# Kernel tuning notes

Hardware: AMD Instinct MI355X
Metric: run time of the kernel (lower is better)

## Reference

```python
import jax, jax.numpy as jnp
import numpy as np

EPS = 1e-12   # F.normalize default eps
TH = 0.5      # forward-arg default threshold
CLAMP_LO, CLAMP_HI = 0.01, 0.999


def setup_inputs() -> dict:
    key = jax.random.key(0)
    k1, k2 = jax.random.split(key)
    # x4: ResNet layer3 features after ala1 scaling + upfeat, stride-16 of a 1024px image
    x4 = jax.random.normal(k1, (8, 1024, 64, 64), dtype=jnp.float32)
    # logits: classifier output after upfeat, same spatial grid, 21 classes
    logits = jax.random.normal(k2, (8, 21, 64, 64), dtype=jnp.float32)
    return {"x4": x4, "logits": logits, "pcm": 2}


def reference(x4, logits, pcm):
    b, c, h, w = x4.shape
    hw = h * w
    xf = x4.reshape(b, c, hw)                      # [b, c, hw]
    # F.normalize(dim=1): x / max(||x||_2, eps)
    norm = jnp.sqrt(jnp.sum(xf * xf, axis=1, keepdims=True))
    xn = xf / jnp.maximum(norm, EPS)
    # pixel affinity: [b, hw, hw]
    aff = jnp.einsum('bci,bcj->bij', xn, xn)
    aff = jnp.clip(aff, CLAMP_LO, CLAMP_HI)
    aff = jnp.where(aff < TH, jnp.zeros((), aff.dtype), aff)
    # column-normalize (torch sum over dim=1)
    aff = aff / jnp.sum(aff, axis=1, keepdims=True)
    lf = logits.reshape(b, -1, hw)                 # [b, K, hw]
    for _ in range(pcm):                           # pcm is a Python int
        lf = jnp.einsum('bki,bij->bkj', lf, aff)
    return lf.reshape(b, -1, h, w)
```

## Files before the change

### kernel.cpp

```cpp
#include <hip/hip_runtime.h>
#include <hip/hip_bf16.h>

#define B_   8
#define C_   1024
#define HW_  4096
#define NK   21
#define NT   32
#define NTRI (NT * (NT + 1) / 2)

using bf16 = __hip_bfloat16;
typedef __attribute__((ext_vector_type(4))) float float4_;
typedef __attribute__((ext_vector_type(8))) int int8v;

#define WAITV0() asm volatile("s_waitcnt vmcnt(0)" ::: "memory")
#define FENCE()  asm volatile("" ::: "memory")
#define BARRIER() do { FENCE(); __builtin_amdgcn_s_barrier(); FENCE(); } while (0)

__global__ __launch_bounds__(256) void ktrans(const float* __restrict__ x4, float* __restrict__ sumsq,
                                              unsigned char* __restrict__ Xq, float* __restrict__ colsum) {
    int jt = blockIdx.x, b = blockIdx.y;
    int j0 = jt * 64;
    int t = threadIdx.x;
    __shared__ float tin[128][33];
    __shared__ unsigned int outw[32][260];
    __shared__ float ssq[32];

    if (t < 64) colsum[b * HW_ + j0 + t] = 0.f;

    int jl = t & 31, cl = t >> 5;
    int qq = t >> 5, jq = t & 31;

    for (int jg = 0; jg < 2; ++jg) {
        int jbase = j0 + jg * 32;
        if (t < 32) ssq[t] = 0.f;
        float part = 0.f;

        for (int ct = 0; ct < 8; ++ct) {
            __syncthreads();
#pragma unroll
            for (int cc = 0; cc < 16; ++cc) {
                float v = x4[((size_t)b * C_ + ct * 128 + cc * 8 + cl) * HW_ + jbase + jl];
                tin[cc * 8 + cl][jl] = v;
                part = fmaf(v, v, part);
            }
            __syncthreads();
            unsigned int wv[4];
#pragma unroll
            for (int g = 0; g < 4; ++g) {
                float f0 = tin[qq * 16 + g * 4 + 0][jq];
                float f1 = tin[qq * 16 + g * 4 + 1][jq];
                float f2 = tin[qq * 16 + g * 4 + 2][jq];
                float f3 = tin[qq * 16 + g * 4 + 3][jq];
                unsigned int r = 0;
                r = __builtin_amdgcn_cvt_pk_fp8_f32(f0, f1, r, false);
                r = __builtin_amdgcn_cvt_pk_fp8_f32(f2, f3, r, true);
                wv[g] = r;
            }
            *(uint4*)&outw[jq][ct * 32 + qq * 4] = make_uint4(wv[0], wv[1], wv[2], wv[3]);
        }
        atomicAdd(&ssq[jl], part);
        __syncthreads();

#pragma unroll
        for (int ps = 0; ps < 8; ++ps) {
            int r = ps * 4 + (t >> 6);
            int ch = t & 63;
            uint4 v = *(const uint4*)&outw[r][ch * 4];
            *(uint4*)(Xq + ((size_t)b * HW_ + jbase + r) * C_ + ch * 16) = v;
        }
        if (t < 32) sumsq[b * HW_ + jbase + t] = ssq[t];
        __syncthreads();
    }
}

__global__ __launch_bounds__(256, 2) void kgram(const unsigned char* __restrict__ Xq,
                                                const float* __restrict__ sumsq, bf16* __restrict__ aff,
                                                float* __restrict__ colsum, int* __restrict__ flags) {
    int lin = blockIdx.x;
    int b = lin & 7;
    int p = lin >> 3;
    int it = (int)((2.0f * NT + 1.0f - sqrtf((2.0f * NT + 1.0f) * (2.0f * NT + 1.0f) - 8.0f * (float)p)) * 0.5f);
    while (it > 0 && p < it * NT - it * (it - 1) / 2) --it;
    while (p >= (it + 1) * NT - (it + 1) * it / 2) ++it;
    int jt = it + p - (it * NT - it * (it - 1) / 2);

    int i0 = it * 128, j0 = jt * 128;
    int tid = threadIdx.x, w = tid >> 6, l = tid & 63;
    int wr = w >> 1, wc = w & 1;
    int lrow = l & 15, lk = l >> 4;

    __shared__ __align__(16) unsigned char smem[2][32768];
    __shared__ int fl;

    const unsigned char* XA = Xq + ((size_t)b * HW_ + i0) * C_;
    const unsigned char* XB = Xq + ((size_t)b * HW_ + j0) * C_;

    int rhi = tid >> 3, sl = tid & 7;

    auto stg = [&](unsigned char* buf, int k0) {
#pragma unroll
        for (int q = 0; q < 4; ++q) {
            int R = q * 32 + rhi;
            int gp = sl ^ (R & 7);
            __builtin_amdgcn_global_load_lds(
                (const __attribute__((address_space(1))) void*)(XA + (size_t)R * C_ + k0 + (gp << 4)),
                (__attribute__((address_space(3))) void*)(buf + R * 128 + (sl << 4)), 16, 0, 0);
            __builtin_amdgcn_global_load_lds(
                (const __attribute__((address_space(1))) void*)(XB + (size_t)R * C_ + k0 + (gp << 4)),
                (__attribute__((address_space(3))) void*)(buf + 16384 + R * 128 + (sl << 4)), 16, 0, 0);
        }
    };

    auto ldfrag = [&](const unsigned char* base, int r) {
        int sw = r & 7;
        uint4 lo = *(const uint4*)(base + r * 128 + (((lk * 2) ^ sw) << 4));
        uint4 hi = *(const uint4*)(base + r * 128 + (((lk * 2 + 1) ^ sw) << 4));
        int8v v; v[0] = lo.x; v[1] = lo.y; v[2] = lo.z; v[3] = lo.w;
        v[4] = hi.x; v[5] = hi.y; v[6] = hi.z; v[7] = hi.w;
        return v;
    };

    float4_ acc[4][4];
#pragma unroll
    for (int m = 0; m < 4; ++m)
#pragma unroll
        for (int n = 0; n < 4; ++n) acc[m][n] = {0.f, 0.f, 0.f, 0.f};

    stg(smem[0], 0);
    WAITV0();
    BARRIER();

    for (int kt = 0; kt < 8; ++kt) {
        unsigned char* cur = smem[kt & 1];
        if (kt < 7) stg(smem[(kt + 1) & 1], (kt + 1) * 128);

        int8v bv[4];
#pragma unroll
        for (int n = 0; n < 4; ++n) bv[n] = ldfrag(cur + 16384, wc * 64 + n * 16 + lrow);
        __builtin_amdgcn_s_setprio(1);
#pragma unroll
        for (int m = 0; m < 4; ++m) {
            int8v av = ldfrag(cur, wr * 64 + m * 16 + lrow);
#pragma unroll
            for (int n = 0; n < 4; ++n)
                acc[m][n] = __builtin_amdgcn_mfma_scale_f32_16x16x128_f8f6f4(
                    av, bv[n], acc[m][n], 0, 0, 0, 0x7f7f7f7f, 0, 0x7f7f7f7f);
        }
        __builtin_amdgcn_s_setprio(0);

        if (kt < 7) WAITV0();
        BARRIER();
    }

    float rnj[4];
#pragma unroll
    for (int n = 0; n < 4; ++n) {
        int j = j0 + wc * 64 + n * 16 + lrow;
        rnj[n] = 1.0f / fmaxf(sqrtf(sumsq[b * HW_ + j]), 1e-12f);
    }
    float rni[4][4];
#pragma unroll
    for (int m = 0; m < 4; ++m)
#pragma unroll
        for (int r = 0; r < 4; ++r) {
            int i = i0 + wr * 64 + m * 16 + lk * 4 + r;
            rni[m][r] = 1.0f / fmaxf(sqrtf(sumsq[b * HW_ + i]), 1e-12f);
        }
    bool any = false;
#pragma unroll
    for (int m = 0; m < 4; ++m)
#pragma unroll
        for (int n = 0; n < 4; ++n)
#pragma unroll
            for (int r = 0; r < 4; ++r) {
                acc[m][n][r] *= rni[m][r] * rnj[n];
                any |= (acc[m][n][r] >= 0.5f);
            }

    if (tid == 0) fl = 0;
    __syncthreads();
    unsigned long long bal = __ballot(any);
    if (l == 0 && bal != 0ull) atomicOr(&fl, 1);
    __syncthreads();
    bool mirror = (it != jt);
    if (tid == 0) {
        flags[(b * NT + it) * NT + jt] = fl;
        if (mirror) flags[(b * NT + jt) * NT + it] = fl;
    }

    if (fl) {
        size_t affb = (size_t)b * HW_ * HW_;
        float rsum[4][4];
#pragma unroll
        for (int m = 0; m < 4; ++m)
#pragma unroll
            for (int r = 0; r < 4; ++r) rsum[m][r] = 0.f;

#pragma unroll
        for (int n = 0; n < 4; ++n) {
            int j = j0 + wc * 64 + n * 16 + lrow;
            float cs = 0.f;
#pragma unroll
            for (int m = 0; m < 4; ++m) {
#pragma unroll
                for (int r = 0; r < 4; ++r) {
                    float v = acc[m][n][r];
                    v = fminf(fmaxf(v, 0.01f), 0.999f);
                    v = (v < 0.5f) ? 0.0f : v;
                    bf16 bb = __float2bfloat16(v);
                    int i = i0 + wr * 64 + m * 16 + lk * 4 + r;
                    aff[affb + (size_t)i * HW_ + j] = bb;
                    float bf = __bfloat162float(bb);
                    cs += bf;
                    rsum[m][r] += bf;
                    if (mirror) aff[affb + (size_t)j * HW_ + i] = bb;
                }
            }
            cs += __shfl_xor(cs, 16);
            cs += __shfl_xor(cs, 32);
            if (lk == 0) atomicAdd(&colsum[b * HW_ + j], cs);
        }
        if (mirror) {
#pragma unroll
            for (int m = 0; m < 4; ++m) {
#pragma unroll
                for (int r = 0; r < 4; ++r) {
                    float s = rsum[m][r];
                    s += __shfl_xor(s, 1);
                    s += __shfl_xor(s, 2);
                    s += __shfl_xor(s, 4);
                    s += __shfl_xor(s, 8);
                    if (lrow == 0) {
                        int i = i0 + wr * 64 + m * 16 + lk * 4 + r;
                        atomicAdd(&colsum[b * HW_ + i], s);
                    }
                }
            }
        }
    }
}

__global__ __launch_bounds__(256) void kprop2(const float* __restrict__ lf, const bf16* __restrict__ aff,
                                              const int* __restrict__ flags, const float* __restrict__ colsum,
                                              float* __restrict__ outp) {
    int jt = blockIdx.x, b = blockIdx.y;
    int t = threadIdx.x;
    int q = t >> 7, jl = t & 127;
    int j = jt * 128 + jl;
    __shared__ float lfs[NK * 128];
    __shared__ float lf1t[NK * 128];

    float oacc[NK];
#pragma unroll
    for (int k = 0; k < NK; ++k) oacc[k] = 0.f;

    for (int it = 0; it < NT; ++it) {
        if (flags[(b * NT + it) * NT + jt] == 0) continue;

        float racc[NK];
#pragma unroll
        for (int k = 0; k < NK; ++k) racc[k] = 0.f;

        for (int ht = 0; ht < NT; ++ht) {
            if (flags[(b * NT + ht) * NT + it] == 0) continue;
            __syncthreads();
            for (int idx = t; idx < NK * 128; idx += 256)
                lfs[idx] = lf[((size_t)b * NK + (idx >> 7)) * HW_ + ht * 128 + (idx & 127)];
            __syncthreads();
            const bf16* ap = aff + ((size_t)b * HW_ + ht * 128 + q * 64) * HW_ + it * 128 + jl;
            for (int ii = 0; ii < 64; ii += 4) {
                float a0 = __bfloat162float(ap[(size_t)(ii + 0) * HW_]);
                float a1 = __bfloat162float(ap[(size_t)(ii + 1) * HW_]);
                float a2 = __bfloat162float(ap[(size_t)(ii + 2) * HW_]);
                float a3 = __bfloat162float(ap[(size_t)(ii + 3) * HW_]);
                int base = q * 64 + ii;
#pragma unroll
                for (int k = 0; k < NK; ++k)
                    racc[k] = fmaf(lfs[(k << 7) + base + 0], a0,
                               fmaf(lfs[(k << 7) + base + 1], a1,
                               fmaf(lfs[(k << 7) + base + 2], a2,
                               fmaf(lfs[(k << 7) + base + 3], a3, racc[k]))));
            }
        }
        __syncthreads();
        if (q == 1) {
#pragma unroll
            for (int k = 0; k < NK; ++k) lfs[(k << 7) + jl] = racc[k];
        }
        __syncthreads();
        if (q == 0) {
            float invi = 1.0f / colsum[b * HW_ + it * 128 + jl];
#pragma unroll
            for (int k = 0; k < NK; ++k)
                lf1t[(k << 7) + jl] = (racc[k] + lfs[(k << 7) + jl]) * invi;
        }
        __syncthreads();

        const bf16* ap2 = aff + ((size_t)b * HW_ + it * 128 + q * 64) * HW_ + j;
        for (int ii = 0; ii < 64; ii += 4) {
            float a0 = __bfloat162float(ap2[(size_t)(ii + 0) * HW_]);
            float a1 = __bfloat162float(ap2[(size_t)(ii + 1) * HW_]);
            float a2 = __bfloat162float(ap2[(size_t)(ii + 2) * HW_]);
            float a3 = __bfloat162float(ap2[(size_t)(ii + 3) * HW_]);
            int base = q * 64 + ii;
#pragma unroll
            for (int k = 0; k < NK; ++k)
                oacc[k] = fmaf(lf1t[(k << 7) + base + 0], a0,
                           fmaf(lf1t[(k << 7) + base + 1], a1,
                           fmaf(lf1t[(k << 7) + base + 2], a2,
                           fmaf(lf1t[(k << 7) + base + 3], a3, oacc[k]))));
        }
    }

    __syncthreads();
    if (q == 1) {
#pragma unroll
        for (int k = 0; k < NK; ++k) lfs[(k << 7) + jl] = oacc[k];
    }
    __syncthreads();
    if (q == 0) {
        float inv = 1.0f / colsum[b * HW_ + j];
#pragma unroll
        for (int k = 0; k < NK; ++k)
            outp[((size_t)b * NK + k) * HW_ + j] = (oacc[k] + lfs[(k << 7) + jl]) * inv;
    }
}

extern "C" void kernel_launch(void* const* d_in, const int* in_sizes, int n_in,
                              void* d_out, int out_size, void* d_ws, size_t ws_size,
                              hipStream_t stream) {
    const float* x4 = (const float*)d_in[0];
    const float* logits = (const float*)d_in[1];
    float* out = (float*)d_out;

    char* w = (char*)d_ws;
    size_t off = 0;
    auto take = [&](size_t bytes) {
        char* p = w + off;
        off += (bytes + 255) & ~(size_t)255;
        return p;
    };
    unsigned char* Xq = (unsigned char*)take((size_t)B_ * HW_ * C_);
    bf16* aff     = (bf16*)take((size_t)B_ * HW_ * HW_ * 2);
    float* colsum = (float*)take((size_t)B_ * HW_ * 4);
    int*   flags  = (int*)take((size_t)B_ * NT * NT * 4);
    float* sumsq  = (float*)take((size_t)B_ * HW_ * 4);

    ktrans<<<dim3(64, B_), dim3(256), 0, stream>>>(x4, sumsq, Xq, colsum);
    kgram <<<dim3(NTRI * B_), dim3(256), 0, stream>>>(Xq, sumsq, aff, colsum, flags);
    kprop2<<<dim3(NT, B_), dim3(256), 0, stream>>>(logits, aff, flags, colsum, out);
}
```

Baseline: 336.5 us.

## Switch Gram kernel to 32x32x64 FP8 MFMA with smaller K tiles

The Gram kernel now uses 32x32x64 scaled FP8 MFMA with a 2x2 accumulator grid per wave instead of 4x4 tiles of 16x16x128. K staging drops to 64-byte slices over 16 iterations, which halves LDS per block and raises the launch-bounds occupancy hint from 2 to 4. Inverse norms are computed once in the transpose kernel rather than per Gram block. The epilogue row and column reductions are rewritten for the new accumulator layout. The cost is more loop iterations and barriers, and possibly more register pressure under the higher occupancy target.

```diff
diff --git a/kernel.cpp b/kernel.cpp
--- a/kernel.cpp
+++ b/kernel.cpp
@@ -9,14 +9,14 @@
 #define NTRI (NT * (NT + 1) / 2)
 
 using bf16 = __hip_bfloat16;
-typedef __attribute__((ext_vector_type(4))) float float4_;
+typedef __attribute__((ext_vector_type(16))) float f32x16;
 typedef __attribute__((ext_vector_type(8))) int int8v;
 
 #define WAITV0() asm volatile("s_waitcnt vmcnt(0)" ::: "memory")
 #define FENCE()  asm volatile("" ::: "memory")
 #define BARRIER() do { FENCE(); __builtin_amdgcn_s_barrier(); FENCE(); } while (0)
 
-__global__ __launch_bounds__(256) void ktrans(const float* __restrict__ x4, float* __restrict__ sumsq,
+__global__ __launch_bounds__(256) void ktrans(const float* __restrict__ x4, float* __restrict__ rn,
                                               unsigned char* __restrict__ Xq, float* __restrict__ colsum) {
     int jt = blockIdx.x, b = blockIdx.y;
     int j0 = jt * 64;
@@ -68,13 +68,13 @@
             uint4 v = *(const uint4*)&outw[r][ch * 4];
             *(uint4*)(Xq + ((size_t)b * HW_ + jbase + r) * C_ + ch * 16) = v;
         }
-        if (t < 32) sumsq[b * HW_ + jbase + t] = ssq[t];
+        if (t < 32) rn[b * HW_ + jbase + t] = 1.0f / fmaxf(sqrtf(ssq[t]), 1e-12f);
         __syncthreads();
     }
 }
 
-__global__ __launch_bounds__(256, 2) void kgram(const unsigned char* __restrict__ Xq,
-                                                const float* __restrict__ sumsq, bf16* __restrict__ aff,
+__global__ __launch_bounds__(256, 4) void kgram(const unsigned char* __restrict__ Xq,
+                                                const float* __restrict__ rn, bf16* __restrict__ aff,
                                                 float* __restrict__ colsum, int* __restrict__ flags) {
     int lin = blockIdx.x;
     int b = lin & 7;
@@ -87,95 +87,91 @@
     int i0 = it * 128, j0 = jt * 128;
     int tid = threadIdx.x, w = tid >> 6, l = tid & 63;
     int wr = w >> 1, wc = w & 1;
-    int lrow = l & 15, lk = l >> 4;
-
-    __shared__ __align__(16) unsigned char smem[2][32768];
+    int lc = l & 31, hi = l >> 5;
+
+    __shared__ __align__(16) unsigned char smem[2][16384];
     __shared__ int fl;
 
     const unsigned char* XA = Xq + ((size_t)b * HW_ + i0) * C_;
     const unsigned char* XB = Xq + ((size_t)b * HW_ + j0) * C_;
 
-    int rhi = tid >> 3, sl = tid & 7;
+    int rlo = tid >> 2, sl = tid & 3;
 
     auto stg = [&](unsigned char* buf, int k0) {
 #pragma unroll
-        for (int q = 0; q < 4; ++q) {
-            int R = q * 32 + rhi;
-            int gp = sl ^ (R & 7);
+        for (int q = 0; q < 2; ++q) {
+            int R = q * 64 + rlo;
+            int gp = sl ^ ((R >> 1) & 3);
             __builtin_amdgcn_global_load_lds(
                 (const __attribute__((address_space(1))) void*)(XA + (size_t)R * C_ + k0 + (gp << 4)),
-                (__attribute__((address_space(3))) void*)(buf + R * 128 + (sl << 4)), 16, 0, 0);
+                (__attribute__((address_space(3))) void*)(buf + R * 64 + (sl << 4)), 16, 0, 0);
             __builtin_amdgcn_global_load_lds(
                 (const __attribute__((address_space(1))) void*)(XB + (size_t)R * C_ + k0 + (gp << 4)),
-                (__attribute__((address_space(3))) void*)(buf + 16384 + R * 128 + (sl << 4)), 16, 0, 0);
+                (__attribute__((address_space(3))) void*)(buf + 8192 + R * 64 + (sl << 4)), 16, 0, 0);
         }
     };
 
     auto ldfrag = [&](const unsigned char* base, int r) {
-        int sw = r & 7;
-        uint4 lo = *(const uint4*)(base + r * 128 + (((lk * 2) ^ sw) << 4));
-        uint4 hi = *(const uint4*)(base + r * 128 + (((lk * 2 + 1) ^ sw) << 4));
+        int sw = (r >> 1) & 3;
+        uint4 lo = *(const uint4*)(base + r * 64 + (((hi * 2) ^ sw) << 4));
+        uint4 hh = *(const uint4*)(base + r * 64 + (((hi * 2 + 1) ^ sw) << 4));
         int8v v; v[0] = lo.x; v[1] = lo.y; v[2] = lo.z; v[3] = lo.w;
-        v[4] = hi.x; v[5] = hi.y; v[6] = hi.z; v[7] = hi.w;
+        v[4] = hh.x; v[5] = hh.y; v[6] = hh.z; v[7] = hh.w;
         return v;
     };
 
-    float4_ acc[4][4];
-#pragma unroll
-    for (int m = 0; m < 4; ++m)
-#pragma unroll
-        for (int n = 0; n < 4; ++n) acc[m][n] = {0.f, 0.f, 0.f, 0.f};
+    f32x16 acc[2][2];
+#pragma unroll
+    for (int m = 0; m < 2; ++m)
+#pragma unroll
+        for (int n = 0; n < 2; ++n)
+#pragma unroll
+            for (int r = 0; r < 16; ++r) acc[m][n][r] = 0.f;
 
     stg(smem[0], 0);
     WAITV0();
     BARRIER();
 
-    for (int kt = 0; kt < 8; ++kt) {
+    for (int kt = 0; kt < 16; ++kt) {
         unsigned char* cur = smem[kt & 1];
-        if (kt < 7) stg(smem[(kt + 1) & 1], (kt + 1) * 128);
-
-        int8v bv[4];
-#pragma unroll
-        for (int n = 0; n < 4; ++n) bv[n] = ldfrag(cur + 16384, wc * 64 + n * 16 + lrow);
+        if (kt < 15) stg(smem[(kt + 1) & 1], (kt + 1) * 64);
+
+        int8v bv[2];
+#pragma unroll
+        for (int n = 0; n < 2; ++n) bv[n] = ldfrag(cur + 8192, wc * 64 + n * 32 + lc);
         __builtin_amdgcn_s_setprio(1);
 #pragma unroll
-        for (int m = 0; m < 4; ++m) {
-            int8v av = ldfrag(cur, wr * 64 + m * 16 + lrow);
-#pragma unroll
-            for (int n = 0; n < 4; ++n)
-                acc[m][n] = __builtin_amdgcn_mfma_scale_f32_16x16x128_f8f6f4(
+        for (int m = 0; m < 2; ++m) {
+            int8v av = ldfrag(cur, wr * 64 + m * 32 + lc);
+#pragma unroll
+            for (int n = 0; n < 2; ++n)
+                acc[m][n] = __builtin_amdgcn_mfma_scale_f32_32x32x64_f8f6f4(
                     av, bv[n], acc[m][n], 0, 0, 0, 0x7f7f7f7f, 0, 0x7f7f7f7f);
         }
         __builtin_amdgcn_s_setprio(0);
 
-        if (kt < 7) WAITV0();
+        if (kt < 15) WAITV0();
         BARRIER();
     }
 
-    float rnj[4];
-#pragma unroll
-    for (int n = 0; n < 4; ++n) {
-        int j = j0 + wc * 64 + n * 16 + lrow;
-        rnj[n] = 1.0f / fmaxf(sqrtf(sumsq[b * HW_ + j]), 1e-12f);
-    }
-    float rni[4][4];
-#pragma unroll
-    for (int m = 0; m < 4; ++m)
-#pragma unroll
-        for (int r = 0; r < 4; ++r) {
-            int i = i0 + wr * 64 + m * 16 + lk * 4 + r;
-            rni[m][r] = 1.0f / fmaxf(sqrtf(sumsq[b * HW_ + i]), 1e-12f);
-        }
+    float rnj[2];
+#pragma unroll
+    for (int n = 0; n < 2; ++n)
+        rnj[n] = rn[b * HW_ + j0 + wc * 64 + n * 32 + lc];
+
     bool any = false;
 #pragma unroll
-    for (int m = 0; m < 4; ++m)
-#pragma unroll
-        for (int n = 0; n < 4; ++n)
-#pragma unroll
-            for (int r = 0; r < 4; ++r) {
-                acc[m][n][r] *= rni[m][r] * rnj[n];
-                any |= (acc[m][n][r] >= 0.5f);
-            }
+    for (int m = 0; m < 2; ++m)
+#pragma unroll
+        for (int reg = 0; reg < 16; ++reg) {
+            int rr = (reg & 3) + 4 * hi + 8 * (reg >> 2);
+            float rni = rn[b * HW_ + i0 + wr * 64 + m * 32 + rr];
+#pragma unroll
+            for (int n = 0; n < 2; ++n) {
+                acc[m][n][reg] *= rni * rnj[n];
+                any |= (acc[m][n][reg] >= 0.5f);
+            }
+        }
 
     if (tid == 0) fl = 0;
     __syncthreads();
@@ -190,52 +186,53 @@
 
     if (fl) {
         size_t affb = (size_t)b * HW_ * HW_;
-        float rsum[4][4];
-#pragma unroll
-        for (int m = 0; m < 4; ++m)
-#pragma unroll
-            for (int r = 0; r < 4; ++r) rsum[m][r] = 0.f;
-
-#pragma unroll
-        for (int n = 0; n < 4; ++n) {
-            int j = j0 + wc * 64 + n * 16 + lrow;
-            float cs = 0.f;
-#pragma unroll
-            for (int m = 0; m < 4; ++m) {
-#pragma unroll
-                for (int r = 0; r < 4; ++r) {
-                    float v = acc[m][n][r];
+        float csn[2] = {0.f, 0.f};
+
+#pragma unroll
+        for (int m = 0; m < 2; ++m) {
+            float rs[16];
+#pragma unroll
+            for (int r = 0; r < 16; ++r) rs[r] = 0.f;
+
+#pragma unroll
+            for (int n = 0; n < 2; ++n) {
+                int j = j0 + wc * 64 + n * 32 + lc;
+#pragma unroll
+                for (int reg = 0; reg < 16; ++reg) {
+                    float v = acc[m][n][reg];
                     v = fminf(fmaxf(v, 0.01f), 0.999f);
                     v = (v < 0.5f) ? 0.0f : v;
                     bf16 bb = __float2bfloat16(v);
-                    int i = i0 + wr * 64 + m * 16 + lk * 4 + r;
+                    int rr = (reg & 3) + 4 * hi + 8 * (reg >> 2);
+                    int i = i0 + wr * 64 + m * 32 + rr;
                     aff[affb + (size_t)i * HW_ + j] = bb;
                     float bf = __bfloat162float(bb);
-                    cs += bf;
-                    rsum[m][r] += bf;
+                    csn[n] += bf;
+                    rs[reg] += bf;
                     if (mirror) aff[affb + (size_t)j * HW_ + i] = bb;
                 }
             }
-            cs += __shfl_xor(cs, 16);
-            cs += __shfl_xor(cs, 32);
-            if (lk == 0) atomicAdd(&colsum[b * HW_ + j], cs);
-        }
-        if (mirror) {
-#pragma unroll
-            for (int m = 0; m < 4; ++m) {
-#pragma unroll
-                for (int r = 0; r < 4; ++r) {
-                    float s = rsum[m][r];
+            if (mirror) {
+#pragma unroll
+                for (int reg = 0; reg < 16; ++reg) {
+                    float s = rs[reg];
                     s += __shfl_xor(s, 1);
                     s += __shfl_xor(s, 2);
                     s += __shfl_xor(s, 4);
                     s += __shfl_xor(s, 8);
-                    if (lrow == 0) {
-                        int i = i0 + wr * 64 + m * 16 + lk * 4 + r;
-                        atomicAdd(&colsum[b * HW_ + i], s);
+                    s += __shfl_xor(s, 16);
+                    if (lc == 0) {
+                        int rr = (reg & 3) + 4 * hi + 8 * (reg >> 2);
+                        atomicAdd(&colsum[b * HW_ + i0 + wr * 64 + m * 32 + rr], s);
                     }
                 }
             }
+        }
+#pragma unroll
+        for (int n = 0; n < 2; ++n) {
+            float cs = csn[n];
+            cs += __shfl_xor(cs, 32);
+            if (hi == 0) atomicAdd(&colsum[b * HW_ + j0 + wc * 64 + n * 32 + lc], cs);
         }
     }
 }
@@ -344,9 +341,9 @@
     bf16* aff     = (bf16*)take((size_t)B_ * HW_ * HW_ * 2);
     float* colsum = (float*)take((size_t)B_ * HW_ * 4);
     int*   flags  = (int*)take((size_t)B_ * NT * NT * 4);
-    float* sumsq  = (float*)take((size_t)B_ * HW_ * 4);
-
-    ktrans<<<dim3(64, B_), dim3(256), 0, stream>>>(x4, sumsq, Xq, colsum);
-    kgram <<<dim3(NTRI * B_), dim3(256), 0, stream>>>(Xq, sumsq, aff, colsum, flags);
+    float* rn     = (float*)take((size_t)B_ * HW_ * 4);
+
+    ktrans<<<dim3(64, B_), dim3(256), 0, stream>>>(x4, rn, Xq, colsum);
+    kgram <<<dim3(NTRI * B_), dim3(256), 0, stream>>>(Xq, rn, aff, colsum, flags);
     kprop2<<<dim3(NT, B_), dim3(256), 0, stream>>>(logits, aff, flags, colsum, out);
 }
```

After: 329.8 us. -2.0%, faster.
